# Performance work log

Measured on AMD Instinct MI355X. Metric: run time of the kernel, lower is better.

Reference implementation:

```python
import jax, jax.numpy as jnp
import numpy as np

B, L, D_MODEL = 2, 2048, 1024
D_INNER, D_STATE, DT_RANK, D_CONV = 2048, 16, 64, 4
EPS = 1e-5


def setup_inputs() -> dict:
    key = jax.random.key(0)
    ks = jax.random.split(key, 12)
    s = lambda fan: 1.0 / np.sqrt(fan)
    return {
        "x": jax.random.normal(ks[0], (B, L, D_MODEL), jnp.float32),
        "norm_w": jnp.ones((D_MODEL,), jnp.float32),
        "W_in": jax.random.normal(ks[1], (2 * D_INNER, D_MODEL), jnp.float32) * s(D_MODEL),
        "W_conv": jax.random.normal(ks[2], (D_INNER, D_CONV), jnp.float32) * s(D_CONV),
        "b_conv": jnp.zeros((D_INNER,), jnp.float32),
        "W_xproj": jax.random.normal(ks[3], (DT_RANK + 2 * D_STATE, D_INNER), jnp.float32) * s(D_INNER),
        "W_dt": jax.random.normal(ks[4], (D_INNER, DT_RANK), jnp.float32) * s(DT_RANK),
        "b_dt": jax.random.normal(ks[5], (D_INNER,), jnp.float32) * 0.1,
        # A initialized as log(1..d_state) per channel (standard Mamba S4D-real init)
        "A_log": jnp.log(jnp.broadcast_to(jnp.arange(1, D_STATE + 1, dtype=jnp.float32), (D_INNER, D_STATE))),
        "D": jnp.ones((D_INNER,), jnp.float32),
        "W_out": jax.random.normal(ks[6], (D_MODEL, D_INNER), jnp.float32) * s(D_INNER),
    }


def _mamba_residual(x, norm_w, W_in, W_conv, b_conv, W_xproj, W_dt, b_dt, A_log, D, W_out):
    # RMSNorm
    xn = x * jax.lax.rsqrt(jnp.mean(x * x, axis=-1, keepdims=True) + EPS) * norm_w
    # in_proj -> split into u (ssm branch) and z (gate)
    xz = jnp.einsum("bld,ed->ble", xn, W_in)            # [b, l, 2*d_inner]
    u, z = jnp.split(xz, 2, axis=-1)                     # each [b, l, d_inner]
    # depthwise causal conv1d over time
    u_t = jnp.transpose(u, (0, 2, 1))                    # [b, d_inner, l]
    u_c = jax.lax.conv_general_dilated(
        u_t, W_conv[:, None, :], window_strides=(1,),
        padding=[(D_CONV - 1, 0)], feature_group_count=D_INNER,
        dimension_numbers=("NCH", "OIH", "NCH"))
    u_c = jax.nn.silu(u_c + b_conv[None, :, None])       # [b, d_inner, l]
    u = jnp.transpose(u_c, (0, 2, 1))                    # [b, l, d_inner]
    # x_proj -> (dt, B, C)
    x_dbl = jnp.einsum("bld,ed->ble", u, W_xproj)        # [b, l, dt_rank+2n]
    dt, Bm, Cm = jnp.split(x_dbl, [DT_RANK, DT_RANK + D_STATE], axis=-1)
    dt = jax.nn.softplus(jnp.einsum("blr,dr->bld", dt, W_dt) + b_dt)  # [b, l, d_inner]
    A = -jnp.exp(A_log)                                  # [d_inner, n]

    # selective scan over time
    def step(h, ins):
        dt_t, B_t, C_t, u_t = ins                        # [b,d],[b,n],[b,n],[b,d]
        dA = jnp.exp(dt_t[..., None] * A)                # [b, d, n]
        h = dA * h + (dt_t * u_t)[..., None] * B_t[:, None, :]
        y = jnp.einsum("bdn,bn->bd", h, C_t)
        return h, y

    h0 = jnp.zeros((x.shape[0], D_INNER, D_STATE), x.dtype)
    ins = (jnp.transpose(dt, (1, 0, 2)), jnp.transpose(Bm, (1, 0, 2)),
           jnp.transpose(Cm, (1, 0, 2)), jnp.transpose(u, (1, 0, 2)))
    _, ys = jax.lax.scan(step, h0, ins)                  # [l, b, d_inner]
    y = jnp.transpose(ys, (1, 0, 2)) + u * D             # [b, l, d_inner]
    y = y * jax.nn.silu(z)
    out = jnp.einsum("ble,de->bld", y, W_out)
    return out + x  # residual (block_mode 'residual'/'none')


def reference(x, norm_w, W_in, W_conv, b_conv, W_xproj, W_dt, b_dt, A_log, D, W_out):
    return _mamba_residual(x, norm_w, W_in, W_conv, b_conv, W_xproj, W_dt, b_dt, A_log, D, W_out)
```

## Files before the change

### kernel.cpp

```cpp
#include <hip/hip_runtime.h>

typedef unsigned short u16;
typedef unsigned int u32;
typedef short bf16x8 __attribute__((ext_vector_type(8)));
typedef float f32x4 __attribute__((ext_vector_type(4)));

static constexpr int LS = 2048;
static constexpr int DM = 1024;
static constexpr int DI = 2048;
static constexpr int DSn = 16;
static constexpr int DTRk = 64;
static constexpr int MR = 4096;
static constexpr int NCH = 64;
static constexpr int CL = LS / NCH;
static constexpr float L2E = 1.44269504f;

#define DEV __device__ __forceinline__

DEV u16 f2bf(float f) {
  u32 u = __float_as_uint(f);
  u32 r = (u + 0x7FFF + ((u >> 16) & 1)) >> 16;
  return (u16)r;
}
DEV float bf2f(u16 h) { return __uint_as_float(((u32)h) << 16); }

DEV void gload16(const u16* g, u16* l) {
  __builtin_amdgcn_global_load_lds((const __attribute__((address_space(1))) u32*)g,
                                   (__attribute__((address_space(3))) u32*)l, 16, 0, 0);
}

DEV void bar() { asm volatile("s_barrier" ::: "memory"); }

#define CALC_POWERS(dst, basev)                                              \
  do {                                                                       \
    const float e1_ = (basev);                                               \
    const float e2_ = e1_ * e1_, e3_ = e2_ * e1_, e4_ = e2_ * e2_;           \
    const float e5_ = e4_ * e1_, e6_ = e4_ * e2_, e7_ = e4_ * e3_,           \
                e8_ = e4_ * e4_;                                             \
    dst[0] = e1_; dst[1] = e2_; dst[2] = e3_; dst[3] = e4_;                  \
    dst[4] = e5_; dst[5] = e6_; dst[6] = e7_; dst[7] = e8_;                  \
    dst[8] = e8_ * e1_;  dst[9] = e8_ * e2_;  dst[10] = e8_ * e3_;           \
    dst[11] = e8_ * e4_; dst[12] = e8_ * e5_; dst[13] = e8_ * e6_;           \
    dst[14] = e8_ * e7_; dst[15] = e8_ * e8_;                                \
  } while (0)

__global__ __launch_bounds__(256) void cvt_weights(const float* __restrict__ W_in,
                                                   const float* __restrict__ W_out,
                                                   const float* __restrict__ W_dt,
                                                   const float* __restrict__ W_xp,
                                                   u16* __restrict__ Win_b,
                                                   u16* __restrict__ Wout_b,
                                                   u16* __restrict__ Wdt_b,
                                                   u16* __restrict__ Wxp_b) {
  const int N0 = 4096 * 1024;
  const int N1 = N0 + 1024 * 2048;
  const int N2 = N1 + 2048 * 64;
  const int N3 = N2 + 128 * 2048;
  int i = blockIdx.x * 256 + threadIdx.x;
  const int stride = gridDim.x * 256;
  for (; i < N3; i += stride) {
    if (i < N0) {
      Win_b[i] = f2bf(W_in[i]);
    } else if (i < N1) {
      const int j = i - N0; Wout_b[j] = f2bf(W_out[j]);
    } else if (i < N2) {
      const int j = i - N1; Wdt_b[j] = f2bf(W_dt[j]);
    } else {
      const int j = i - N2; const int r = j >> 11, c = j & 2047;
      Wxp_b[j] = (r < 96) ? f2bf(W_xp[r * 2048 + c]) : (u16)0;
    }
  }
}

__global__ __launch_bounds__(256) void rmsnorm_kernel(const float* __restrict__ x,
                                                      const float* __restrict__ w,
                                                      u16* __restrict__ xn) {
  const int row = blockIdx.x;
  const int tid = threadIdx.x;
  const float4 v = reinterpret_cast<const float4*>(x + (size_t)row * DM)[tid];
  float ss = v.x * v.x + v.y * v.y + v.z * v.z + v.w * v.w;
#pragma unroll
  for (int o = 32; o; o >>= 1) ss += __shfl_xor(ss, o);
  __shared__ float red[4];
  if ((tid & 63) == 0) red[tid >> 6] = ss;
  __syncthreads();
  const float tot = red[0] + red[1] + red[2] + red[3];
  const float scale = rsqrtf(tot * (1.0f / DM) + 1e-5f);
  const float4 wv = reinterpret_cast<const float4*>(w)[tid];
  ushort4 o4;
  o4.x = f2bf(v.x * scale * wv.x);
  o4.y = f2bf(v.y * scale * wv.y);
  o4.z = f2bf(v.z * scale * wv.z);
  o4.w = f2bf(v.w * scale * wv.w);
  *reinterpret_cast<ushort4*>(&xn[(size_t)row * DM + tid * 4]) = o4;
}

DEV void stage_op(const u16* __restrict__ P, int K, int rowbase, int k0,
                  u16* dst, int tid) {
#pragma unroll
  for (int i = 0; i < 4; ++i) {
    const int row = i * 64 + (tid >> 3);
    const int slot = (tid & 7) ^ (row & 7);
    gload16(P + (size_t)(rowbase + row) * K + k0 + slot * 8, dst + i * 4096 + tid * 8);
  }
}

#define ISS_A(dst, off, MH) do { \
  _Pragma("unroll") for (int m_ = 0; m_ < 4; ++m_) \
  _Pragma("unroll") for (int kk_ = 0; kk_ < 2; ++kk_) \
    dst[m_ * 2 + kk_] = *reinterpret_cast<const bf16x8*>( \
        &Asl[(off) + wr * 8192 + ((MH) * 64 + m_ * 16 + lrow) * 64 + ((kk_ * 4 + kq) ^ rsw) * 8]); \
} while (0)

#define ISS_B(dst, off, NH) do { \
  _Pragma("unroll") for (int n_ = 0; n_ < 2; ++n_) \
  _Pragma("unroll") for (int kk_ = 0; kk_ < 2; ++kk_) \
    dst[n_ * 2 + kk_] = *reinterpret_cast<const bf16x8*>( \
        &Bsl[(off) + bh * 8192 + (bq * 64 + ((NH) * 2 + n_) * 16 + lrow) * 64 + ((kk_ * 4 + kq) ^ rsw) * 8]); \
} while (0)

#define MMAQ(areg, breg, MH, NH) do { \
  __builtin_amdgcn_s_setprio(1); \
  _Pragma("unroll") for (int m_ = 0; m_ < 4; ++m_) \
  _Pragma("unroll") for (int n_ = 0; n_ < 2; ++n_) \
  _Pragma("unroll") for (int kk_ = 0; kk_ < 2; ++kk_) \
    acc[(MH) * 4 + m_][(NH) * 2 + n_] = __builtin_amdgcn_mfma_f32_16x16x32_bf16( \
        areg[m_ * 2 + kk_], breg[n_ * 2 + kk_], acc[(MH) * 4 + m_][(NH) * 2 + n_], 0, 0, 0); \
  __builtin_amdgcn_s_setprio(0); \
} while (0)

template <int EPI>
__global__ __launch_bounds__(512, 2) void gemm256(const u16* __restrict__ A,
                                                  const u16* __restrict__ Bw,
                                                  int M, int N, int K, int Klen,
                                                  u16* __restrict__ outB,
                                                  float* __restrict__ outF) {
  __shared__ __align__(16) u16 Asl[2 * 16384];
  __shared__ __align__(16) u16 Bsl[2 * 16384];
  const int tid = threadIdx.x;
  const int lane = tid & 63;
  const int wid = tid >> 6;
  const int wr = wid >> 2;
  const int wc = wid & 3;
  const int lrow = lane & 15;
  const int kq = lane >> 4;
  const int rsw = lane & 7;
  const int bh = wc >> 1, bq = wc & 1;

  const int nwg = gridDim.x * gridDim.y;
  int wg = blockIdx.y * gridDim.x + blockIdx.x;
  wg = (wg & 7) * (nwg >> 3) + (wg >> 3);
  const int bn = (wg % gridDim.x) * 256;
  const int bm = (wg / gridDim.x) * 256;
  const int koff = blockIdx.z * Klen;

  const int nt = Klen >> 6;

  f32x4 acc[8][4] = {};
  bf16x8 aX[8], aY[8], bX[4], bY[4];

  stage_op(A, K, bm, koff, &Asl[0], tid);
  stage_op(Bw, K, bn, koff, &Bsl[0], tid);
  stage_op(A, K, bm, koff + 64, &Asl[16384], tid);
  stage_op(Bw, K, bn, koff + 64, &Bsl[16384], tid);
  asm volatile("s_waitcnt vmcnt(8)" ::: "memory");
  bar();
  ISS_A(aX, 0, 0);
  ISS_B(bX, 0, 0);

  for (int I = 0; I < (nt >> 1); ++I) {
    const int u = 2 * I;
    ISS_B(bY, 0, 1);
    MMAQ(aX, bX, 0, 0);
    ISS_A(aY, 0, 1);
    MMAQ(aX, bY, 0, 1);
    MMAQ(aY, bX, 1, 0);
    asm volatile("s_waitcnt vmcnt(0)" ::: "memory");
    bar();
    if (u + 2 < nt) {
      stage_op(A, K, bm, koff + (u + 2) * 64, &Asl[0], tid);
      stage_op(Bw, K, bn, koff + (u + 2) * 64, &Bsl[0], tid);
    }
    ISS_A(aX, 16384, 0);
    ISS_B(bX, 16384, 0);
    MMAQ(aY, bY, 1, 1);
    ISS_B(bY, 16384, 1);
    MMAQ(aX, bX, 0, 0);
    ISS_A(aY, 16384, 1);
    MMAQ(aX, bY, 0, 1);
    MMAQ(aY, bX, 1, 0);
    asm volatile("s_waitcnt vmcnt(0)" ::: "memory");
    bar();
    if (u + 3 < nt) {
      stage_op(A, K, bm, koff + (u + 3) * 64, &Asl[16384], tid);
      stage_op(Bw, K, bn, koff + (u + 3) * 64, &Bsl[16384], tid);
    }
    if (u + 2 < nt) {
      ISS_A(aX, 0, 0);
      ISS_B(bX, 0, 0);
    }
    MMAQ(aY, bY, 1, 1);
  }

  if (EPI == 0) {
#pragma unroll
    for (int m = 0; m < 8; ++m)
#pragma unroll
      for (int n = 0; n < 4; ++n) {
        const int col = bn + wc * 64 + n * 16 + lrow;
#pragma unroll
        for (int rr = 0; rr < 4; ++rr) {
          const int row = bm + wr * 128 + m * 16 + kq * 4 + rr;
          outB[(size_t)row * N + col] = f2bf(acc[m][n][rr]);
        }
      }
  } else {
    float* dstF = outF + (size_t)blockIdx.z * MR * N;
#pragma unroll
    for (int m = 0; m < 8; ++m)
#pragma unroll
      for (int n = 0; n < 4; ++n) {
        const int col = bn + wc * 64 + n * 16 + lrow;
#pragma unroll
        for (int rr = 0; rr < 4; ++rr) {
          const int row = bm + wr * 128 + m * 16 + kq * 4 + rr;
          dstF[(size_t)row * N + col] = acc[m][n][rr];
        }
      }
  }
}

__global__ __launch_bounds__(256) void outproj_reduce4(const float* __restrict__ p,
                                                       const float* __restrict__ x,
                                                       float* __restrict__ out) {
  const int id = blockIdx.x * 256 + threadIdx.x;
  float4 o = reinterpret_cast<const float4*>(x)[id];
#pragma unroll
  for (int s = 0; s < 4; ++s) {
    const float4 a = reinterpret_cast<const float4*>(p + (size_t)s * MR * 1024)[id];
    o.x += a.x; o.y += a.y; o.z += a.z; o.w += a.w;
  }
  reinterpret_cast<float4*>(out)[id] = o;
}

__global__ __launch_bounds__(256) void gemm_dt(const u16* __restrict__ A,
                                               const u16* __restrict__ Bw,
                                               int M, int N, int K,
                                               u16* __restrict__ outB,
                                               const float* __restrict__ aux) {
  __shared__ __align__(16) u16 As[128 * 32];
  __shared__ __align__(16) u16 Bs[128 * 32];
  const int tid = threadIdx.x;
  const int lane = tid & 63;
  const int wid = tid >> 6;
  const int wr = wid >> 1, wc = wid & 1;
  const int nwg = gridDim.x * gridDim.y;
  int wg = blockIdx.y * gridDim.x + blockIdx.x;
  wg = (wg & 7) * (nwg >> 3) + (wg >> 3);
  const int bn = (wg % gridDim.x) * 128;
  const int bm = (wg / gridDim.x) * 128;
  const int r0 = tid >> 2;
  const int c0 = (tid & 3) * 8;
  const int lrow = lane & 15, kq = lane >> 4;

  f32x4 acc[4][4] = {};

  const u16* Ab = A + (size_t)bm * K;
  const u16* Bb = Bw + (size_t)bn * K;

  for (int k0 = 0; k0 < K; k0 += 32) {
    gload16(Ab + (size_t)r0 * K + k0 + c0, &As[r0 * 32 + c0]);
    gload16(Ab + (size_t)(r0 + 64) * K + k0 + c0, &As[(r0 + 64) * 32 + c0]);
    gload16(Bb + (size_t)r0 * K + k0 + c0, &Bs[r0 * 32 + c0]);
    gload16(Bb + (size_t)(r0 + 64) * K + k0 + c0, &Bs[(r0 + 64) * 32 + c0]);
    __syncthreads();
    bf16x8 af[4], bfr[4];
#pragma unroll
    for (int m = 0; m < 4; ++m)
      af[m] = *reinterpret_cast<const bf16x8*>(&As[(wr * 64 + m * 16 + lrow) * 32 + kq * 8]);
#pragma unroll
    for (int n = 0; n < 4; ++n)
      bfr[n] = *reinterpret_cast<const bf16x8*>(&Bs[(wc * 64 + n * 16 + lrow) * 32 + kq * 8]);
#pragma unroll
    for (int m = 0; m < 4; ++m)
#pragma unroll
      for (int n = 0; n < 4; ++n)
        acc[m][n] = __builtin_amdgcn_mfma_f32_16x16x32_bf16(af[m], bfr[n], acc[m][n], 0, 0, 0);
    __syncthreads();
  }

#pragma unroll
  for (int m = 0; m < 4; ++m) {
#pragma unroll
    for (int n = 0; n < 4; ++n) {
      const int col = bn + wc * 64 + n * 16 + lrow;
#pragma unroll
      for (int r = 0; r < 4; ++r) {
        const int row = bm + wr * 64 + m * 16 + kq * 4 + r;
        const float xv = acc[m][n][r] + aux[col];
        const float sp = fmaxf(xv, 0.f) + log1pf(__expf(-fabsf(xv)));
        outB[(size_t)row * N + col] = f2bf(sp);
      }
    }
  }
}

__global__ __launch_bounds__(256) void gemm_xproj_splitk(const u16* __restrict__ A,
                                                         const u16* __restrict__ Bw,
                                                         float* __restrict__ p0,
                                                         float* __restrict__ p1) {
  __shared__ __align__(16) u16 As[128 * 32];
  __shared__ __align__(16) u16 Bs[128 * 32];
  const int tid = threadIdx.x;
  const int lane = tid & 63;
  const int wid = tid >> 6;
  const int wr = wid >> 1, wc = wid & 1;
  const int kp = blockIdx.x;
  const int bm = blockIdx.y * 128;
  const int koff = kp * 256;
  const int r0 = tid >> 2;
  const int c0 = (tid & 3) * 8;
  const int lrow = lane & 15, kq = lane >> 4;

  f32x4 acc[4][4] = {};
  const u16* Ab = A + (size_t)bm * DI + koff;
  const u16* Bb = Bw + koff;

  for (int k0 = 0; k0 < 256; k0 += 32) {
    gload16(Ab + (size_t)r0 * DI + k0 + c0, &As[r0 * 32 + c0]);
    gload16(Ab + (size_t)(r0 + 64) * DI + k0 + c0, &As[(r0 + 64) * 32 + c0]);
    gload16(Bb + (size_t)r0 * DI + k0 + c0, &Bs[r0 * 32 + c0]);
    gload16(Bb + (size_t)(r0 + 64) * DI + k0 + c0, &Bs[(r0 + 64) * 32 + c0]);
    __syncthreads();
    bf16x8 af[4], bfr[4];
#pragma unroll
    for (int m = 0; m < 4; ++m)
      af[m] = *reinterpret_cast<const bf16x8*>(&As[(wr * 64 + m * 16 + lrow) * 32 + kq * 8]);
#pragma unroll
    for (int n = 0; n < 4; ++n)
      bfr[n] = *reinterpret_cast<const bf16x8*>(&Bs[(wc * 64 + n * 16 + lrow) * 32 + kq * 8]);
#pragma unroll
    for (int m = 0; m < 4; ++m)
#pragma unroll
      for (int n = 0; n < 4; ++n)
        acc[m][n] = __builtin_amdgcn_mfma_f32_16x16x32_bf16(af[m], bfr[n], acc[m][n], 0, 0, 0);
    __syncthreads();
  }

  float* dst = (kp < 4 ? p0 : p1) + (size_t)(kp & 3) * MR * 128;
#pragma unroll
  for (int m = 0; m < 4; ++m)
#pragma unroll
    for (int n = 0; n < 4; ++n) {
      const int col = wc * 64 + n * 16 + lrow;
#pragma unroll
      for (int r = 0; r < 4; ++r) {
        const int row = bm + wr * 64 + m * 16 + kq * 4 + r;
        dst[(size_t)row * 128 + col] = acc[m][n][r];
      }
    }
}

__global__ __launch_bounds__(256) void xproj_reduce(const float* __restrict__ p0,
                                                    const float* __restrict__ p1,
                                                    float* __restrict__ xdbl,
                                                    u16* __restrict__ dtr) {
  const int id = blockIdx.x * 256 + threadIdx.x;
  const int row = id >> 7, col = id & 127;
  float s = 0.f;
#pragma unroll
  for (int kp = 0; kp < 4; ++kp) s += p0[(size_t)kp * MR * 128 + id];
#pragma unroll
  for (int kp = 0; kp < 4; ++kp) s += p1[(size_t)kp * MR * 128 + id];
  if (col < 96) xdbl[(size_t)row * 96 + col] = s;
  if (col < 64) dtr[(size_t)row * 64 + col] = f2bf(s);
}

__global__ __launch_bounds__(256) void conv_silu_kernel(const u16* __restrict__ xz,
                                                        const float* __restrict__ Wc,
                                                        const float* __restrict__ bc,
                                                        u16* __restrict__ uc) {
  const int id = blockIdx.x * 256 + threadIdx.x;
  const int d8 = id & (DI / 8 - 1);
  const int t = (id >> 8) & (LS - 1);
  const int b = id >> 19;
  const int d0 = d8 * 8;
  const size_t rowb = (size_t)b * LS;
  bf16x8 r[4];
#pragma unroll
  for (int k = 0; k < 4; ++k) {
    const int tt = t - 3 + k;
    if (tt >= 0)
      r[k] = *reinterpret_cast<const bf16x8*>(&xz[(rowb + tt) * (2 * DI) + d0]);
    else
      r[k] = bf16x8{0, 0, 0, 0, 0, 0, 0, 0};
  }
  const float4 bc0 = *reinterpret_cast<const float4*>(&bc[d0]);
  const float4 bc1 = *reinterpret_cast<const float4*>(&bc[d0 + 4]);
  const float bcv[8] = {bc0.x, bc0.y, bc0.z, bc0.w, bc1.x, bc1.y, bc1.z, bc1.w};
  u16 o[8];
#pragma unroll
  for (int j = 0; j < 8; ++j) {
    const float4 w = *reinterpret_cast<const float4*>(&Wc[(d0 + j) * 4]);
    float s = bcv[j];
    s += bf2f((u16)r[0][j]) * w.x;
    s += bf2f((u16)r[1][j]) * w.y;
    s += bf2f((u16)r[2][j]) * w.z;
    s += bf2f((u16)r[3][j]) * w.w;
    const float sl = s / (1.f + __expf(-s));
    o[j] = f2bf(sl);
  }
  *reinterpret_cast<bf16x8*>(&uc[(rowb + t) * DI + d0]) =
      *reinterpret_cast<const bf16x8*>(o);
}


__global__ __launch_bounds__(128, 4) void scan_phase1(const u16* __restrict__ dtb,
                                                      const float* __restrict__ xdbl,
                                                      const u16* __restrict__ uc,
                                                      const float* __restrict__ Alog,
                                                      float* __restrict__ P,
                                                      float* __restrict__ S) {
  __shared__ __align__(16) u16 s_dt[16 * 128];
  __shared__ __align__(16) u16 s_uc[16 * 128];
  __shared__ __align__(16) float s_b[16 * 16];
  const int tid = threadIdx.x;
  const int blk = blockIdx.x;
  const int d0 = (blk & 15) * 128;
  const int c = (blk >> 4) & (NCH - 1);
  const int b = blk >> 10;
  const int d = d0 + tid;
  const size_t tbase = (size_t)b * LS + c * CL;

  float Av[16];
  bool fastA = true;
#pragma unroll
  for (int j = 0; j < 16; j += 4) {
    const float4 Alv = *reinterpret_cast<const float4*>(&Alog[d * DSn + j]);
    Av[j + 0] = -__expf(Alv.x); Av[j + 1] = -__expf(Alv.y);
    Av[j + 2] = -__expf(Alv.z); Av[j + 3] = -__expf(Alv.w);
  }
#pragma unroll
  for (int j = 0; j < 16; ++j)
    fastA = fastA && (fabsf(Av[j] + (float)(j + 1)) < 1e-3f * (float)(j + 1));

  float h[16];
#pragma unroll
  for (int j = 0; j < 16; ++j) h[j] = 0.f;
  float sdt = 0.f;

  for (int w = 0; w < 2; ++w) {
    const size_t twb = tbase + w * 16;
#pragma unroll
    for (int j = 0; j < 2; ++j) {
      const int k = j * 128 + tid;
      const int row = k >> 4, col = (k & 15) * 8;
      gload16(dtb + (twb + row) * DI + d0 + col, &s_dt[row * 128 + col]);
      gload16(uc + (twb + row) * DI + d0 + col, &s_uc[row * 128 + col]);
    }
    if (tid < 64) {
      gload16((const u16*)(xdbl + (twb + (tid >> 2)) * 96 + DTRk + (tid & 3) * 4),
              (u16*)&s_b[tid * 4]);
    }
    __syncthreads();
    if (fastA) {
      for (int tr = 0; tr < 16; ++tr) {
        const float dtv = bf2f(s_dt[tr * 128 + tid]);
        const float uv = bf2f(s_uc[tr * 128 + tid]);
        const float du = dtv * uv;
        sdt += dtv;
        float dA[16];
        CALC_POWERS(dA, exp2f(-L2E * dtv));
        float Bf[16];
#pragma unroll
        for (int j = 0; j < 16; j += 4) {
          const float4 Bv = *reinterpret_cast<const float4*>(&s_b[tr * 16 + j]);
          Bf[j] = Bv.x; Bf[j + 1] = Bv.y; Bf[j + 2] = Bv.z; Bf[j + 3] = Bv.w;
        }
#pragma unroll
        for (int j = 0; j < 16; ++j) h[j] = dA[j] * h[j] + du * Bf[j];
      }
    } else {
      for (int tr = 0; tr < 16; ++tr) {
        const float dtv = bf2f(s_dt[tr * 128 + tid]);
        const float uv = bf2f(s_uc[tr * 128 + tid]);
        const float du = dtv * uv;
        sdt += dtv;
        float Bf[16];
#pragma unroll
        for (int j = 0; j < 16; j += 4) {
          const float4 Bv = *reinterpret_cast<const float4*>(&s_b[tr * 16 + j]);
          Bf[j] = Bv.x; Bf[j + 1] = Bv.y; Bf[j + 2] = Bv.z; Bf[j + 3] = Bv.w;
        }
#pragma unroll
        for (int j = 0; j < 16; ++j)
          h[j] = exp2f(dtv * Av[j] * L2E) * h[j] + du * Bf[j];
      }
    }
    __syncthreads();
  }

  const size_t oi = (((size_t)b * NCH + c) * DI + d) * DSn;
  float Pw[16];
  if (fastA) {
    CALC_POWERS(Pw, exp2f(-L2E * sdt));
  } else {
#pragma unroll
    for (int j = 0; j < 16; ++j) Pw[j] = exp2f(Av[j] * L2E * sdt);
  }
#pragma unroll
  for (int j = 0; j < 16; j += 4) {
    float4 Sv = {h[j], h[j + 1], h[j + 2], h[j + 3]};
    float4 Pv = {Pw[j], Pw[j + 1], Pw[j + 2], Pw[j + 3]};
    *reinterpret_cast<float4*>(&S[oi + j]) = Sv;
    *reinterpret_cast<float4*>(&P[oi + j]) = Pv;
  }
}

__global__ __launch_bounds__(256) void scan_phase2(const float* __restrict__ P,
                                                   float* __restrict__ S) {
  const int gid = blockIdx.x * 256 + threadIdx.x;
  const int ng = gid & 3;
  const int d = (gid >> 2) & (DI - 1);
  const int b = gid >> 13;
  float4 h = {0.f, 0.f, 0.f, 0.f};
  for (int cc = 0; cc < NCH; ++cc) {
    const size_t oi = (((size_t)b * NCH + cc) * DI + d) * DSn + ng * 4;
    const float4 Pv = *reinterpret_cast<const float4*>(&P[oi]);
    const float4 Sv = *reinterpret_cast<const float4*>(&S[oi]);
    *reinterpret_cast<float4*>(&S[oi]) = h;
    h.x = Sv.x + Pv.x * h.x;
    h.y = Sv.y + Pv.y * h.y;
    h.z = Sv.z + Pv.z * h.z;
    h.w = Sv.w + Pv.w * h.w;
  }
}

__global__ __launch_bounds__(128, 4) void scan_phase3(const u16* __restrict__ dtb,
                                                      const float* __restrict__ xdbl,
                                                      const u16* __restrict__ uc,
                                                      const u16* __restrict__ xz,
                                                      const float* __restrict__ Alog,
                                                      const float* __restrict__ Dp,
                                                      const float* __restrict__ Hin,
                                                      u16* __restrict__ yb) {
  __shared__ __align__(16) u16 s_dt[16 * 128];
  __shared__ __align__(16) u16 s_uc[16 * 128];
  __shared__ __align__(16) u16 s_z[16 * 128];
  __shared__ __align__(16) float s_bc[16 * 32];
  const int tid = threadIdx.x;
  const int blk = blockIdx.x;
  const int d0 = (blk & 15) * 128;
  const int c = (blk >> 4) & (NCH - 1);
  const int b = blk >> 10;
  const int d = d0 + tid;
  const size_t tbase = (size_t)b * LS + c * CL;

  float Av[16];
  bool fastA = true;
#pragma unroll
  for (int j = 0; j < 16; j += 4) {
    const float4 Alv = *reinterpret_cast<const float4*>(&Alog[d * DSn + j]);
    Av[j + 0] = -__expf(Alv.x); Av[j + 1] = -__expf(Alv.y);
    Av[j + 2] = -__expf(Alv.z); Av[j + 3] = -__expf(Alv.w);
  }
#pragma unroll
  for (int j = 0; j < 16; ++j)
    fastA = fastA && (fabsf(Av[j] + (float)(j + 1)) < 1e-3f * (float)(j + 1));

  const float Dd = Dp[d];
  const size_t oi = (((size_t)b * NCH + c) * DI + d) * DSn;
  float h[16];
#pragma unroll
  for (int j = 0; j < 16; j += 4) {
    const float4 hv = *reinterpret_cast<const float4*>(&Hin[oi + j]);
    h[j] = hv.x; h[j + 1] = hv.y; h[j + 2] = hv.z; h[j + 3] = hv.w;
  }

  for (int w = 0; w < 2; ++w) {
    const size_t twb = tbase + w * 16;
#pragma unroll
    for (int j = 0; j < 2; ++j) {
      const int k = j * 128 + tid;
      const int row = k >> 4, col = (k & 15) * 8;
      gload16(dtb + (twb + row) * DI + d0 + col, &s_dt[row * 128 + col]);
      gload16(uc + (twb + row) * DI + d0 + col, &s_uc[row * 128 + col]);
      gload16(xz + (twb + row) * (2 * DI) + DI + d0 + col, &s_z[row * 128 + col]);
    }
    {
      gload16((const u16*)(xdbl + (twb + (tid >> 3)) * 96 + DTRk + (tid & 7) * 4),
              (u16*)&s_bc[tid * 4]);
    }
    __syncthreads();
#define P3_STEP(DA_STMT)                                                        \
    for (int tr = 0; tr < 16; ++tr) {                                           \
      const float dtv = bf2f(s_dt[tr * 128 + tid]);                             \
      const float uv = bf2f(s_uc[tr * 128 + tid]);                              \
      const float du = dtv * uv;                                                \
      float dA[16];                                                             \
      DA_STMT;                                                                  \
      float Bf[16], Cf[16];                                                     \
      _Pragma("unroll")                                                         \
      for (int j = 0; j < 16; j += 4) {                                         \
        const float4 Bv = *reinterpret_cast<const float4*>(&s_bc[tr * 32 + j]); \
        const float4 Cv = *reinterpret_cast<const float4*>(&s_bc[tr * 32 + 16 + j]); \
        Bf[j] = Bv.x; Bf[j + 1] = Bv.y; Bf[j + 2] = Bv.z; Bf[j + 3] = Bv.w;     \
        Cf[j] = Cv.x; Cf[j + 1] = Cv.y; Cf[j + 2] = Cv.z; Cf[j + 3] = Cv.w;     \
      }                                                                         \
      _Pragma("unroll")                                                         \
      for (int j = 0; j < 16; ++j) h[j] = dA[j] * h[j] + du * Bf[j];            \
      float y0 = 0.f, y1 = 0.f, y2 = 0.f, y3 = 0.f;                             \
      _Pragma("unroll")                                                         \
      for (int j = 0; j < 16; j += 4) {                                         \
        y0 += h[j] * Cf[j];                                                     \
        y1 += h[j + 1] * Cf[j + 1];                                             \
        y2 += h[j + 2] * Cf[j + 2];                                             \
        y3 += h[j + 3] * Cf[j + 3];                                             \
      }                                                                         \
      const float y = (y0 + y1) + (y2 + y3) + uv * Dd;                          \
      const float z = bf2f(s_z[tr * 128 + tid]);                                \
      const float sz = z / (1.f + __expf(-z));                                  \
      yb[(twb + tr) * DI + d] = f2bf(y * sz);                                   \
    }
    if (fastA) {
      P3_STEP(CALC_POWERS(dA, exp2f(-L2E * dtv)));
    } else {
      P3_STEP({ _Pragma("unroll") for (int j = 0; j < 16; ++j) dA[j] = exp2f(dtv * Av[j] * L2E); });
    }
#undef P3_STEP
    __syncthreads();
  }
}

extern "C" void kernel_launch(void* const* d_in, const int* in_sizes, int n_in,
                              void* d_out, int out_size, void* d_ws, size_t ws_size,
                              hipStream_t stream) {
  (void)in_sizes; (void)n_in; (void)out_size; (void)ws_size;
  const float* x      = (const float*)d_in[0];
  const float* norm_w = (const float*)d_in[1];
  const float* W_in   = (const float*)d_in[2];
  const float* W_conv = (const float*)d_in[3];
  const float* b_conv = (const float*)d_in[4];
  const float* W_xp   = (const float*)d_in[5];
  const float* W_dt   = (const float*)d_in[6];
  const float* b_dt   = (const float*)d_in[7];
  const float* A_log  = (const float*)d_in[8];
  const float* Dvec   = (const float*)d_in[9];
  const float* W_out  = (const float*)d_in[10];
  float* out = (float*)d_out;

  char* ws = (char*)d_ws;
  size_t off = 0;
  auto alloc = [&](size_t bytes) -> void* {
    void* p = ws + off;
    off += (bytes + 255) & ~(size_t)255;
    return p;
  };
  u16* Win_b  = (u16*)alloc((size_t)4096 * 1024 * 2);
  u16* Wout_b = (u16*)alloc((size_t)1024 * 2048 * 2);
  u16* Wxp_b  = (u16*)alloc((size_t)128 * 2048 * 2);
  u16* Wdt_b  = (u16*)alloc((size_t)2048 * 64 * 2);
  u16* xn_b   = (u16*)alloc((size_t)MR * DM * 2);
  u16* xz_b   = (u16*)alloc((size_t)MR * 2 * DI * 2);
  u16* uc_b   = (u16*)alloc((size_t)MR * DI * 2);
  float* xdbl = (float*)alloc((size_t)MR * 96 * 4);
  u16* dtr_b  = (u16*)alloc((size_t)MR * 64 * 2);
  u16* dtf_b  = (u16*)alloc((size_t)MR * DI * 2);
  u16* y_b    = (u16*)alloc((size_t)MR * DI * 2);
  float* Sbuf = (float*)alloc((size_t)2 * NCH * DI * DSn * 4);
  float* part0 = (float*)Win_b;
  float* part1 = (float*)xn_b;
  float* Pbuf = (float*)y_b;
  float* opart = (float*)xz_b;

  cvt_weights<<<2048, 256, 0, stream>>>(W_in, W_out, W_dt, W_xp,
                                        Win_b, Wout_b, Wdt_b, Wxp_b);

  rmsnorm_kernel<<<MR, 256, 0, stream>>>(x, norm_w, xn_b);

  gemm256<0><<<dim3(16, 16, 1), 512, 0, stream>>>(xn_b, Win_b, MR, 4096, 1024, 1024,
                                                  xz_b, nullptr);
  conv_silu_kernel<<<4096, 256, 0, stream>>>(xz_b, W_conv, b_conv, uc_b);
  gemm_xproj_splitk<<<dim3(8, 32), 256, 0, stream>>>(uc_b, Wxp_b, part0, part1);
  xproj_reduce<<<2048, 256, 0, stream>>>(part0, part1, xdbl, dtr_b);
  gemm_dt<<<dim3(16, 32), 256, 0, stream>>>(dtr_b, Wdt_b, MR, 2048, 64, dtf_b, b_dt);
  scan_phase1<<<2048, 128, 0, stream>>>(dtf_b, xdbl, uc_b, A_log, Pbuf, Sbuf);
  scan_phase2<<<64, 256, 0, stream>>>(Pbuf, Sbuf);
  scan_phase3<<<2048, 128, 0, stream>>>(dtf_b, xdbl, uc_b, xz_b, A_log, Dvec,
                                        Sbuf, y_b);
  gemm256<1><<<dim3(4, 16, 4), 512, 0, stream>>>(y_b, Wout_b, MR, 1024, 2048, 512,
                                                 nullptr, opart);
  outproj_reduce4<<<4096, 256, 0, stream>>>(opart, x, out);
}
```

Before: 251.1 us.

## Restructure GEMM main loop into single-stage prefetch with sched barriers

Replaces the hand-interleaved two-tile software pipeline, which prefetched two K-tiles ahead with register double-buffering across tiles, with a simpler loop. Each iteration prefetches the next tile into the alternate LDS buffer, then loads fragments from the current buffer and runs the four MFMA quadrants, separated by scheduling barriers. A and B tiles are merged into one shared array. The aim is to cut register pressure and scheduling complexity, at the cost of less overlap between LDS reads and MFMAs across tiles and a barrier every tile.

```diff
diff --git a/kernel.cpp b/kernel.cpp
--- a/kernel.cpp
+++ b/kernel.cpp
@@ -109,14 +109,14 @@
   _Pragma("unroll") for (int m_ = 0; m_ < 4; ++m_) \
   _Pragma("unroll") for (int kk_ = 0; kk_ < 2; ++kk_) \
     dst[m_ * 2 + kk_] = *reinterpret_cast<const bf16x8*>( \
-        &Asl[(off) + wr * 8192 + ((MH) * 64 + m_ * 16 + lrow) * 64 + ((kk_ * 4 + kq) ^ rsw) * 8]); \
+        &SL[(off) + wr * 8192 + ((MH) * 64 + m_ * 16 + lrow) * 64 + ((kk_ * 4 + kq) ^ rsw) * 8]); \
 } while (0)
 
 #define ISS_B(dst, off, NH) do { \
   _Pragma("unroll") for (int n_ = 0; n_ < 2; ++n_) \
   _Pragma("unroll") for (int kk_ = 0; kk_ < 2; ++kk_) \
     dst[n_ * 2 + kk_] = *reinterpret_cast<const bf16x8*>( \
-        &Bsl[(off) + bh * 8192 + (bq * 64 + ((NH) * 2 + n_) * 16 + lrow) * 64 + ((kk_ * 4 + kq) ^ rsw) * 8]); \
+        &SL[(off) + 16384 + bh * 8192 + (bq * 64 + ((NH) * 2 + n_) * 16 + lrow) * 64 + ((kk_ * 4 + kq) ^ rsw) * 8]); \
 } while (0)
 
 #define MMAQ(areg, breg, MH, NH) do { \
@@ -135,8 +135,7 @@
                                                   int M, int N, int K, int Klen,
                                                   u16* __restrict__ outB,
                                                   float* __restrict__ outF) {
-  __shared__ __align__(16) u16 Asl[2 * 16384];
-  __shared__ __align__(16) u16 Bsl[2 * 16384];
+  __shared__ __align__(16) u16 SL[2 * 32768];
   const int tid = threadIdx.x;
   const int lane = tid & 63;
   const int wid = tid >> 6;
@@ -157,49 +156,35 @@
   const int nt = Klen >> 6;
 
   f32x4 acc[8][4] = {};
-  bf16x8 aX[8], aY[8], bX[4], bY[4];
-
-  stage_op(A, K, bm, koff, &Asl[0], tid);
-  stage_op(Bw, K, bn, koff, &Bsl[0], tid);
-  stage_op(A, K, bm, koff + 64, &Asl[16384], tid);
-  stage_op(Bw, K, bn, koff + 64, &Bsl[16384], tid);
-  asm volatile("s_waitcnt vmcnt(8)" ::: "memory");
+  bf16x8 a0[8], a1[8], b0[4], b1[4];
+
+  stage_op(A, K, bm, koff, &SL[0], tid);
+  stage_op(Bw, K, bn, koff, &SL[16384], tid);
+  asm volatile("s_waitcnt vmcnt(0)" ::: "memory");
   bar();
-  ISS_A(aX, 0, 0);
-  ISS_B(bX, 0, 0);
-
-  for (int I = 0; I < (nt >> 1); ++I) {
-    const int u = 2 * I;
-    ISS_B(bY, 0, 1);
-    MMAQ(aX, bX, 0, 0);
-    ISS_A(aY, 0, 1);
-    MMAQ(aX, bY, 0, 1);
-    MMAQ(aY, bX, 1, 0);
-    asm volatile("s_waitcnt vmcnt(0)" ::: "memory");
-    bar();
-    if (u + 2 < nt) {
-      stage_op(A, K, bm, koff + (u + 2) * 64, &Asl[0], tid);
-      stage_op(Bw, K, bn, koff + (u + 2) * 64, &Bsl[0], tid);
-    }
-    ISS_A(aX, 16384, 0);
-    ISS_B(bX, 16384, 0);
-    MMAQ(aY, bY, 1, 1);
-    ISS_B(bY, 16384, 1);
-    MMAQ(aX, bX, 0, 0);
-    ISS_A(aY, 16384, 1);
-    MMAQ(aX, bY, 0, 1);
-    MMAQ(aY, bX, 1, 0);
-    asm volatile("s_waitcnt vmcnt(0)" ::: "memory");
-    bar();
-    if (u + 3 < nt) {
-      stage_op(A, K, bm, koff + (u + 3) * 64, &Asl[16384], tid);
-      stage_op(Bw, K, bn, koff + (u + 3) * 64, &Bsl[16384], tid);
-    }
-    if (u + 2 < nt) {
-      ISS_A(aX, 0, 0);
-      ISS_B(bX, 0, 0);
-    }
-    MMAQ(aY, bY, 1, 1);
+
+  for (int t = 0; t < nt; ++t) {
+    const int cs = (t & 1) * 32768;
+    const int ns = ((t + 1) & 1) * 32768;
+    if (t + 1 < nt) {
+      stage_op(A, K, bm, koff + (t + 1) * 64, &SL[ns], tid);
+      stage_op(Bw, K, bn, koff + (t + 1) * 64, &SL[ns + 16384], tid);
+    }
+    ISS_A(a0, cs, 0);
+    ISS_B(b0, cs, 0);
+    MMAQ(a0, b0, 0, 0);
+    __builtin_amdgcn_sched_barrier(0);
+    ISS_B(b1, cs, 1);
+    MMAQ(a0, b1, 0, 1);
+    __builtin_amdgcn_sched_barrier(0);
+    ISS_A(a1, cs, 1);
+    MMAQ(a1, b0, 1, 0);
+    __builtin_amdgcn_sched_barrier(0);
+    MMAQ(a1, b1, 1, 1);
+    if (t + 1 < nt) {
+      asm volatile("s_waitcnt vmcnt(0)" ::: "memory");
+      bar();
+    }
   }
 
   if (EPI == 0) {
```

Measured after the change: 227.6 us. 1.1x faster.
